# Kernel optimization log

Hardware: AMD Instinct MI355X
Metric: run time of the kernel (lower is better)

The kernel has to match this reference:

```python
import jax, jax.numpy as jnp
import numpy as np

N_NODES = 20000
N_EDGES = 320000
N_GRAPHS = 32
IN_CH = 5
HID = 64
HEADS = 4
DH = HID // HEADS  # 16
LAYERS = 8
EPS = 1e-5
SLOPE = 0.2


def setup_inputs() -> dict:
    key = jax.random.key(0)
    ks = jax.random.split(key, 32)
    inp = {}
    inp['x1'] = jax.random.normal(ks[0], (N_NODES, IN_CH), dtype=jnp.float32)
    inp['x2'] = jax.random.normal(ks[1], (N_NODES, IN_CH), dtype=jnp.float32)
    inp['edge_index1'] = jax.random.randint(ks[2], (2, N_EDGES), 0, N_NODES, dtype=jnp.int32)
    inp['edge_index2'] = jax.random.randint(ks[3], (2, N_EDGES), 0, N_NODES, dtype=jnp.int32)
    inp['batch1'] = jnp.sort(jax.random.randint(ks[4], (N_NODES,), 0, N_GRAPHS, dtype=jnp.int32))
    inp['batch2'] = jnp.sort(jax.random.randint(ks[5], (N_NODES,), 0, N_GRAPHS, dtype=jnp.int32))
    # node_lin
    inp['Wn'] = jax.random.normal(ks[6], (IN_CH, HID), dtype=jnp.float32) / np.sqrt(IN_CH)
    inp['bnode'] = jnp.zeros((HID,), dtype=jnp.float32)
    # GATv2 layers (stacked over LAYERS)
    s = 1.0 / np.sqrt(HID)
    inp['Wl'] = jax.random.normal(ks[7], (LAYERS, HID, HID), dtype=jnp.float32) * s
    inp['bl'] = jnp.zeros((LAYERS, HID), dtype=jnp.float32)
    inp['Wr'] = jax.random.normal(ks[8], (LAYERS, HID, HID), dtype=jnp.float32) * s
    inp['br'] = jnp.zeros((LAYERS, HID), dtype=jnp.float32)
    inp['att'] = jax.random.normal(ks[9], (LAYERS, HEADS, DH), dtype=jnp.float32) / np.sqrt(DH)
    inp['cbias'] = jnp.zeros((LAYERS, HID), dtype=jnp.float32)
    # batch norms
    inp['gamma'] = jnp.ones((LAYERS, HID), dtype=jnp.float32)
    inp['beta'] = jnp.zeros((LAYERS, HID), dtype=jnp.float32)
    # fc head
    inp['f1w'] = jax.random.normal(ks[10], (2 * HID, 256), dtype=jnp.float32) / np.sqrt(2 * HID)
    inp['f1b'] = jnp.zeros((256,), dtype=jnp.float32)
    inp['f2w'] = jax.random.normal(ks[11], (256, 128), dtype=jnp.float32) / np.sqrt(256)
    inp['f2b'] = jnp.zeros((128,), dtype=jnp.float32)
    inp['f3w'] = jax.random.normal(ks[12], (128, 1), dtype=jnp.float32) / np.sqrt(128)
    inp['f3b'] = jnp.zeros((1,), dtype=jnp.float32)
    return inp


def _gatv2_layer(x, src, dst, Wl, bl, Wr, br, att, bias):
    # x: [N, HID]; src/dst: [E'] (self loops included)
    N = x.shape[0]
    xl = (x @ Wl + bl).reshape(N, HEADS, DH)  # source transform
    xr = (x @ Wr + br).reshape(N, HEADS, DH)  # target transform
    e = jax.nn.leaky_relu(xl[src] + xr[dst], SLOPE)          # [E, H, DH]
    score = jnp.einsum('ehd,hd->eh', e, att)                  # [E, H]
    smax = jax.ops.segment_max(score, dst, num_segments=N)    # [N, H]
    ex = jnp.exp(score - smax[dst])
    denom = jax.ops.segment_sum(ex, dst, num_segments=N)
    alpha = ex / denom[dst]                                   # [E, H]
    msg = alpha[:, :, None] * xl[src]                         # [E, H, DH]
    out = jax.ops.segment_sum(msg, dst, num_segments=N)       # [N, H, DH]
    return out.reshape(N, HID) + bias


def _forward_once(x, edge_index, batch, Wn, bnode, Wl, bl, Wr, br, att, cbias, gamma, beta):
    N = x.shape[0]
    loop = jnp.arange(N, dtype=edge_index.dtype)
    src = jnp.concatenate([edge_index[0], loop])  # add_self_loops=True
    dst = jnp.concatenate([edge_index[1], loop])
    h = x @ Wn + bnode
    for l in range(LAYERS):
        g = _gatv2_layer(h, src, dst, Wl[l], bl[l], Wr[l], br[l], att[l], cbias[l])
        mu = g.mean(axis=0)
        var = g.var(axis=0)
        g = (g - mu) / jnp.sqrt(var + EPS) * gamma[l] + beta[l]
        h = h + jax.nn.elu(g)
    # global_mean_pool
    sums = jax.ops.segment_sum(h, batch, num_segments=N_GRAPHS)
    cnt = jax.ops.segment_sum(jnp.ones((N,), dtype=h.dtype), batch, num_segments=N_GRAPHS)
    return sums / jnp.maximum(cnt, 1.0)[:, None]


def reference(x1, edge_index1, batch1, x2, edge_index2, batch2, Wn, bnode, Wl, bl, Wr, br, att, cbias, gamma, beta, f1w, f1b, f2w, f2b, f3w, f3b):
    o1 = _forward_once(x1, edge_index1, batch1, Wn, bnode, Wl, bl, Wr, br, att, cbias, gamma, beta)
    o2 = _forward_once(x2, edge_index2, batch2, Wn, bnode, Wl, bl, Wr, br, att, cbias, gamma, beta)
    c = jnp.concatenate([o1, o2], axis=1)           # [G, 128]
    h = jax.nn.relu(c @ f1w + f1b)                   # dropout = identity (eval)
    h = jax.nn.relu(h @ f2w + f2b)
    return h @ f3w + f3b                             # [G, 1]
```

## Files before the change

### kernel.cpp

```cpp
#include <hip/hip_runtime.h>
#include <hip/hip_bf16.h>

#define N_NODES 20000
#define HID 64
#define EPS 1e-5f

struct GP {
    const int* ei;
    const int* batch;
    const float* x;
    int* deg;
    int* cursor;
    int* csr;
    float* h;
    float* xl;
    float* xr;
    float* gb;
    float* stats;
    float* osum;
};


__global__ void k_csr_init(GP a, GP b, int n, int two) {
    int t = blockIdx.x * blockDim.x + threadIdx.x;
    if (t < n) {
        a.deg[t] = 1;
        if (two) b.deg[t] = 1;
    }
}

__global__ void k_count(GP a, GP b, int Ea, int Eb, int two) {
    int t = blockIdx.x * blockDim.x + threadIdx.x;
    if (t < Ea) atomicAdd(&a.deg[a.ei[Ea + t]], 1);
    if (two && t < Eb) atomicAdd(&b.deg[b.ei[Eb + t]], 1);
}

#define SCAN_T 1024
#define SCAN_C 20
__global__ __launch_bounds__(1024) void k_scan(GP a, GP b, int n, int totA, int totB) {
    GP g = blockIdx.x ? b : a;
    int total = blockIdx.x ? totB : totA;
    __shared__ int sd[SCAN_T];
    int t = threadIdx.x;
    int base = t * SCAN_C;
    int loc[SCAN_C];
    int s = 0;
#pragma unroll
    for (int i = 0; i < SCAN_C; ++i) {
        int idx = base + i;
        loc[i] = (idx < n) ? g.deg[idx] : 0;
        s += loc[i];
    }
    sd[t] = s;
    __syncthreads();
    for (int off = 1; off < SCAN_T; off <<= 1) {
        int v = (t >= off) ? sd[t - off] : 0;
        __syncthreads();
        sd[t] += v;
        __syncthreads();
    }
    int run = sd[t] - s;
#pragma unroll
    for (int i = 0; i < SCAN_C; ++i) {
        int idx = base + i;
        if (idx < n) { g.deg[idx] = run; g.cursor[idx] = run; run += loc[i]; }
    }
    if (t == 0) g.deg[n] = total;
}

__global__ void k_scatter(GP a, GP b, int Ea, int Eb, int n, int two) {
    int t = blockIdx.x * blockDim.x + threadIdx.x;
    if (t < Ea) {
        int s = a.ei[t], d = a.ei[Ea + t];
        a.csr[atomicAdd(&a.cursor[d], 1)] = s;
    } else if (t < Ea + n) {
        int nn = t - Ea;
        a.csr[atomicAdd(&a.cursor[nn], 1)] = nn;
    }
    if (two) {
        if (t < Eb) {
            int s = b.ei[t], d = b.ei[Eb + t];
            b.csr[atomicAdd(&b.cursor[d], 1)] = s;
        } else if (t < Eb + n) {
            int nn = t - Eb;
            b.csr[atomicAdd(&b.cursor[nn], 1)] = nn;
        }
    }
}


__global__ void k_nodelin(GP a, GP b, int nPer, const float* __restrict__ Wn,
                          const float* __restrict__ bn, int n) {
    int bid = blockIdx.x;
    GP g = a;
    if (bid >= nPer) { g = b; bid -= nPer; }
    int idx = bid * 256 + threadIdx.x;
    if (idx >= n * HID) return;
    int node = idx >> 6, c = idx & 63;
    float acc = bn[c];
#pragma unroll
    for (int k = 0; k < 5; ++k) acc += g.x[node * 5 + k] * Wn[k * HID + c];
    g.h[idx] = acc;
}


__global__ __launch_bounds__(256) void k_lin2(GP ga, GP gbp, int nPer, int n,
        const float* __restrict__ Wl, const float* __restrict__ bl,
        const float* __restrict__ Wr, const float* __restrict__ br,
        const float* __restrict__ gamma, const float* __restrict__ beta, int layer) {
    __shared__ float wls[4096], wrs[4096];
    __shared__ float hs[1024];
    int bid = blockIdx.x;
    GP g = ga;
    if (bid >= nPer) { g = gbp; bid -= nPer; }
    for (int i = threadIdx.x; i < 4096; i += 256) { wls[i] = Wl[i]; wrs[i] = Wr[i]; }
    int c = threadIdx.x & 63;
    int wid = threadIdx.x >> 6;
    float blv = bl[c], brv = br[c];
    float mu = 0.f, inv = 1.f, gam = 1.f, bet = 0.f;
    if (layer > 0) {
        const float* st = g.stats + (layer - 1) * 128;
        float invn = 1.0f / (float)n;
        mu = st[c] * invn;
        float var = st[64 + c] * invn - mu * mu;
        inv = rsqrtf(fmaxf(var, 0.f) + EPS);
        gam = gamma[c]; bet = beta[c];
    }
    int stride = nPer * 16;
    for (int base = bid * 16; base < n; base += stride) {
        int nb = base + wid * 4;
        size_t off = (size_t)nb * 64 + c;
        float h0, h1, h2, h3;
        if (layer > 0) {
            float g0 = g.gb[off], g1 = g.gb[off + 64], g2 = g.gb[off + 128], g3 = g.gb[off + 192];
            float o0 = g.h[off], o1 = g.h[off + 64], o2 = g.h[off + 128], o3 = g.h[off + 192];
            float v0 = (g0 - mu) * inv * gam + bet; v0 = v0 > 0.f ? v0 : expm1f(v0);
            float v1 = (g1 - mu) * inv * gam + bet; v1 = v1 > 0.f ? v1 : expm1f(v1);
            float v2 = (g2 - mu) * inv * gam + bet; v2 = v2 > 0.f ? v2 : expm1f(v2);
            float v3 = (g3 - mu) * inv * gam + bet; v3 = v3 > 0.f ? v3 : expm1f(v3);
            h0 = o0 + v0; h1 = o1 + v1; h2 = o2 + v2; h3 = o3 + v3;
            g.h[off] = h0; g.h[off + 64] = h1; g.h[off + 128] = h2; g.h[off + 192] = h3;
        } else {
            h0 = g.h[off]; h1 = g.h[off + 64]; h2 = g.h[off + 128]; h3 = g.h[off + 192];
        }
        hs[wid * 256 + c] = h0;
        hs[wid * 256 + 64 + c] = h1;
        hs[wid * 256 + 128 + c] = h2;
        hs[wid * 256 + 192 + c] = h3;
        __syncthreads();
        float al0 = blv, al1 = blv, al2 = blv, al3 = blv;
        float ar0 = brv, ar1 = brv, ar2 = brv, ar3 = brv;
        const float* hw = &hs[wid * 256];
#pragma unroll 8
        for (int k = 0; k < 64; ++k) {
            float wl = wls[k * 64 + c], wr = wrs[k * 64 + c];
            float q0 = hw[k], q1 = hw[64 + k], q2 = hw[128 + k], q3 = hw[192 + k];
            al0 += q0 * wl; ar0 += q0 * wr;
            al1 += q1 * wl; ar1 += q1 * wr;
            al2 += q2 * wl; ar2 += q2 * wr;
            al3 += q3 * wl; ar3 += q3 * wr;
        }
        g.xl[off] = al0; g.xl[off + 64] = al1; g.xl[off + 128] = al2; g.xl[off + 192] = al3;
        g.xr[off] = ar0; g.xr[off + 64] = ar1; g.xr[off + 128] = ar2; g.xr[off + 192] = ar3;
        __syncthreads();
    }
}


__device__ __forceinline__ float red16(float p) {
    p += __int_as_float(__builtin_amdgcn_update_dpp(0, __float_as_int(p), 0xB1, 0xF, 0xF, true));
    p += __int_as_float(__builtin_amdgcn_update_dpp(0, __float_as_int(p), 0x4E, 0xF, 0xF, true));
    p += __int_as_float(__builtin_amdgcn_update_dpp(0, __float_as_int(p), 0x141, 0xF, 0xF, true));
    p += __int_as_float(__builtin_amdgcn_update_dpp(0, __float_as_int(p), 0x140, 0xF, 0xF, true));
    return p;
}

__device__ __forceinline__ void upd(float p, float xls, float& m, float& lsum, float& acc) {
    float mn = fmaxf(m, p);
    float sc = __expf(m - mn);
    float wv = __expf(p - mn);
    lsum = lsum * sc + wv;
    acc = acc * sc + wv * xls;
    m = mn;
}

__global__ __launch_bounds__(1024) void k_attn(GP ga, GP gbp, int nPer,
        const float* __restrict__ att, const float* __restrict__ cbias, int layer, int n) {
    int bid = blockIdx.x;
    GP g = ga;
    if (bid >= nPer) { g = gbp; bid -= nPer; }
    int lane = threadIdx.x & 63;
    int wid = threadIdx.x >> 6;
    int gw = bid * 16 + wid;
    int nw = nPer * 16;
    float attv = att[lane];
    float cb = cbias[lane];
    const int* __restrict__ rowptr = g.deg;
    const int* __restrict__ csr = g.csr;
    const float* __restrict__ xl = g.xl;
    const float* __restrict__ xr = g.xr;
    float* __restrict__ gbuf = g.gb;
    float* st = g.stats + layer * 128;
    float bsum = 0.f, bsq = 0.f;
    for (int node = gw; node < n; node += nw) {
        int start = rowptr[node], end = rowptr[node + 1];
        float xrv = xr[(size_t)node * 64 + lane];
        float m = -1e30f, lsum = 0.f, acc = 0.f;
        int idx = start;
        for (; idx + 4 <= end; idx += 4) {
            int s0 = csr[idx], s1 = csr[idx + 1], s2 = csr[idx + 2], s3 = csr[idx + 3];
            float x0 = xl[(size_t)s0 * 64 + lane];
            float x1 = xl[(size_t)s1 * 64 + lane];
            float x2 = xl[(size_t)s2 * 64 + lane];
            float x3 = xl[(size_t)s3 * 64 + lane];
            float e0 = x0 + xrv; e0 = e0 > 0.f ? e0 : 0.2f * e0;
            float e1 = x1 + xrv; e1 = e1 > 0.f ? e1 : 0.2f * e1;
            float e2 = x2 + xrv; e2 = e2 > 0.f ? e2 : 0.2f * e2;
            float e3 = x3 + xrv; e3 = e3 > 0.f ? e3 : 0.2f * e3;
            float p0 = red16(e0 * attv);
            float p1 = red16(e1 * attv);
            float p2 = red16(e2 * attv);
            float p3 = red16(e3 * attv);
            upd(p0, x0, m, lsum, acc);
            upd(p1, x1, m, lsum, acc);
            upd(p2, x2, m, lsum, acc);
            upd(p3, x3, m, lsum, acc);
        }
        for (; idx < end; ++idx) {
            int s0 = csr[idx];
            float x0 = xl[(size_t)s0 * 64 + lane];
            float e0 = x0 + xrv; e0 = e0 > 0.f ? e0 : 0.2f * e0;
            float p0 = red16(e0 * attv);
            upd(p0, x0, m, lsum, acc);
        }
        float outv = acc / lsum + cb;
        gbuf[(size_t)node * 64 + lane] = outv;
        bsum += outv; bsq += outv * outv;
    }
    __shared__ float sred[1024];
    sred[threadIdx.x] = bsum;
    __syncthreads();
    if (threadIdx.x < 64) {
        float t = 0.f;
#pragma unroll
        for (int w = 0; w < 16; ++w) t += sred[w * 64 + threadIdx.x];
        atomicAdd(&st[threadIdx.x], t);
    }
    __syncthreads();
    sred[threadIdx.x] = bsq;
    __syncthreads();
    if (threadIdx.x < 64) {
        float t = 0.f;
#pragma unroll
        for (int w = 0; w < 16; ++w) t += sred[w * 64 + threadIdx.x];
        atomicAdd(&st[64 + threadIdx.x], t);
    }
}


__global__ __launch_bounds__(256) void k_pool(GP ga, GP gbp, int nPer,
        const float* __restrict__ gamma, const float* __restrict__ beta, int n) {
    int bid = blockIdx.x;
    GP g = ga;
    if (bid >= nPer) { g = gbp; bid -= nPer; }
    int lane = threadIdx.x & 63, w = threadIdx.x >> 6;
    const float* st = g.stats + 7 * 128;
    float invn = 1.f / (float)n;
    float mu = st[lane] * invn;
    float var = st[64 + lane] * invn - mu * mu;
    float inv = rsqrtf(fmaxf(var, 0.f) + EPS);
    float gam = gamma[lane], bet = beta[lane];
    int chunk = (n + nPer - 1) / nPer;
    int s = bid * chunk;
    int e = min(s + chunk, n);
    float acc = 0.f;
    int cur = -1;
    for (int node = s + w; node < e; node += 4) {
        int bg = g.batch[node];
        size_t off = (size_t)node * 64 + lane;
        float gv = g.gb[off];
        float hv = g.h[off];
        float v = (gv - mu) * inv * gam + bet;
        float hn = hv + (v > 0.f ? v : expm1f(v));
        if (bg != cur) {
            if (cur >= 0) atomicAdd(&g.osum[cur * 64 + lane], acc);
            acc = 0.f; cur = bg;
        }
        acc += hn;
    }
    if (cur >= 0) atomicAdd(&g.osum[cur * 64 + lane], acc);
}


__device__ __forceinline__ int lb(const int* __restrict__ b, int n, int v) {
    int lo = 0, hi = n;
    while (lo < hi) { int mid = (lo + hi) >> 1; if (b[mid] < v) lo = mid + 1; else hi = mid; }
    return lo;
}

__global__ __launch_bounds__(256) void k_fc(const float* __restrict__ o1, const float* __restrict__ o2,
                                            const int* __restrict__ b1, const int* __restrict__ b2,
                                            const float* __restrict__ f1w, const float* __restrict__ f1b,
                                            const float* __restrict__ f2w, const float* __restrict__ f2b,
                                            const float* __restrict__ f3w, const float* __restrict__ f3b,
                                            float* __restrict__ out, int n) {
    int gid = blockIdx.x, t = threadIdx.x;
    __shared__ float cin[128];
    __shared__ float h1[256];
    __shared__ float red[128];
    __shared__ int cnts[2];
    if (t == 0) cnts[0] = lb(b1, n, gid + 1) - lb(b1, n, gid);
    if (t == 1) cnts[1] = lb(b2, n, gid + 1) - lb(b2, n, gid);
    __syncthreads();
    if (t < 64) {
        float c1 = (float)(cnts[0] > 0 ? cnts[0] : 1);
        float c2 = (float)(cnts[1] > 0 ? cnts[1] : 1);
        cin[t] = o1[gid * 64 + t] / c1;
        cin[64 + t] = o2[gid * 64 + t] / c2;
    }
    __syncthreads();
    float a = f1b[t];
#pragma unroll 8
    for (int k = 0; k < 128; ++k) a += cin[k] * f1w[k * 256 + t];
    h1[t] = fmaxf(a, 0.f);
    __syncthreads();
    if (t < 128) {
        float a2 = f2b[t];
#pragma unroll 8
        for (int k = 0; k < 256; ++k) a2 += h1[k] * f2w[k * 128 + t];
        red[t] = fmaxf(a2, 0.f) * f3w[t];
    }
    __syncthreads();
    for (int off = 64; off > 0; off >>= 1) {
        if (t < off) red[t] += red[t + off];
        __syncthreads();
    }
    if (t == 0) out[gid] = red[0] + f3b[0];
}


extern "C" void kernel_launch(void* const* d_in, const int* in_sizes, int n_in,
                              void* d_out, int out_size, void* d_ws, size_t ws_size,
                              hipStream_t stream) {
    const float* x1 = (const float*)d_in[0];
    const float* x2 = (const float*)d_in[1];
    const int* ei1 = (const int*)d_in[2];
    const int* ei2 = (const int*)d_in[3];
    const int* b1 = (const int*)d_in[4];
    const int* b2 = (const int*)d_in[5];
    const float* Wn = (const float*)d_in[6];
    const float* bnode = (const float*)d_in[7];
    const float* Wl = (const float*)d_in[8];
    const float* bl = (const float*)d_in[9];
    const float* Wr = (const float*)d_in[10];
    const float* br = (const float*)d_in[11];
    const float* att = (const float*)d_in[12];
    const float* cbias = (const float*)d_in[13];
    const float* gamma = (const float*)d_in[14];
    const float* beta = (const float*)d_in[15];
    const float* f1w = (const float*)d_in[16];
    const float* f1b = (const float*)d_in[17];
    const float* f2w = (const float*)d_in[18];
    const float* f2b = (const float*)d_in[19];
    const float* f3w = (const float*)d_in[20];
    const float* f3b = (const float*)d_in[21];
    float* out = (float*)d_out;

    const int N = N_NODES;
    const int EA = in_sizes[2] / 2;
    const int EB = in_sizes[3] / 2;
    const size_t INT_PG = 20096 + 20096 + 340096;
    const size_t BIG = (size_t)N * 64;
    const size_t SMALL = 2 * 1024 + 2 * 2048;
    const size_t dualBytes = 2 * INT_PG * 4 + (8 * BIG + SMALL) * 4;
    const int dual = (ws_size >= dualBytes) ? 1 : 0;

    int* ibase = (int*)d_ws;
    int* iA = ibase;
    int* iB = dual ? ibase + INT_PG : ibase;
    float* fbase = (float*)(ibase + (size_t)(dual ? 2 : 1) * INT_PG);
    float* hA = fbase;
    float* xlA = hA + BIG;
    float* xrA = xlA + BIG;
    float* gbA = xrA + BIG;
    float* hB = dual ? gbA + BIG : hA;
    float* xlB = dual ? hB + BIG : xlA;
    float* xrB = dual ? xlB + BIG : xrA;
    float* gbB = dual ? xrB + BIG : gbA;
    float* small = dual ? gbB + BIG : gbA + BIG;
    float* statsA = small;
    float* statsB = small + 1024;
    float* osumA = small + 2048;
    float* osumB = small + 4096;

    GP A, B;
    A.ei = ei1; A.batch = b1; A.x = x1;
    A.deg = iA; A.cursor = iA + 20096; A.csr = iA + 40192;
    A.h = hA; A.xl = xlA; A.xr = xrA; A.gb = gbA; A.stats = statsA; A.osum = osumA;
    B.ei = ei2; B.batch = b2; B.x = x2;
    B.deg = iB; B.cursor = iB + 20096; B.csr = iB + 40192;
    B.h = hB; B.xl = xlB; B.xr = xrB; B.gb = gbB; B.stats = statsB; B.osum = osumB;

    hipMemsetAsync(small, 0, SMALL * sizeof(float), stream);

    const int LIN2_NB = 625;
    const int ATT_NB = 256;
    const int POOL_NB = 250;

    if (dual) {
        int Emax = EA > EB ? EA : EB;
        k_csr_init<<<(N + 255) / 256, 256, 0, stream>>>(A, B, N, 1);
        k_count<<<(Emax + 255) / 256, 256, 0, stream>>>(A, B, EA, EB, 1);
        k_scan<<<2, 1024, 0, stream>>>(A, B, N, EA + N, EB + N);
        k_scatter<<<(Emax + N + 255) / 256, 256, 0, stream>>>(A, B, EA, EB, N, 1);
        k_nodelin<<<2 * ((N * 64) / 256), 256, 0, stream>>>(A, B, (N * 64) / 256, Wn, bnode, N);
        for (int l = 0; l < 8; ++l) {
            const float* gm = l ? gamma + (l - 1) * 64 : gamma;
            const float* bt = l ? beta + (l - 1) * 64 : beta;
            k_lin2<<<2 * LIN2_NB, 256, 0, stream>>>(A, B, LIN2_NB, N, Wl + l * 4096, bl + l * 64,
                                                    Wr + l * 4096, br + l * 64, gm, bt, l);
            k_attn<<<2 * ATT_NB, 1024, 0, stream>>>(A, B, ATT_NB, att + l * 64, cbias + l * 64, l, N);
        }
        k_pool<<<2 * POOL_NB, 256, 0, stream>>>(A, B, POOL_NB, gamma + 7 * 64, beta + 7 * 64, N);
    } else {
        for (int gi = 0; gi < 2; ++gi) {
            GP G = gi ? B : A;
            int E = gi ? EB : EA;
            k_csr_init<<<(N + 255) / 256, 256, 0, stream>>>(G, G, N, 0);
            k_count<<<(E + 255) / 256, 256, 0, stream>>>(G, G, E, E, 0);
            k_scan<<<1, 1024, 0, stream>>>(G, G, N, E + N, E + N);
            k_scatter<<<(E + N + 255) / 256, 256, 0, stream>>>(G, G, E, E, N, 0);
            k_nodelin<<<(N * 64) / 256, 256, 0, stream>>>(G, G, (N * 64) / 256, Wn, bnode, N);
            for (int l = 0; l < 8; ++l) {
                const float* gm = l ? gamma + (l - 1) * 64 : gamma;
                const float* bt = l ? beta + (l - 1) * 64 : beta;
                k_lin2<<<LIN2_NB, 256, 0, stream>>>(G, G, LIN2_NB, N, Wl + l * 4096, bl + l * 64,
                                                    Wr + l * 4096, br + l * 64, gm, bt, l);
                k_attn<<<ATT_NB, 1024, 0, stream>>>(G, G, ATT_NB, att + l * 64, cbias + l * 64, l, N);
            }
            k_pool<<<POOL_NB, 256, 0, stream>>>(G, G, POOL_NB, gamma + 7 * 64, beta + 7 * 64, N);
        }
    }
    k_fc<<<32, 256, 0, stream>>>(osumA, osumB, b1, b2, f1w, f1b, f2w, f2b, f3w, f3b, out, N);
}
```

Baseline: 749.0 us.

## Replace online softmax with self-loop-anchored exp and retile the lin2 GEMM

In the attention kernel, the running-max online softmax is replaced by a fixed shift: the self-loop score is computed first and every edge weight is exp(min(p - s_self, 80)). This removes the per-edge rescale exps and max tracking, leaving one exp per edge. It risks overflow or precision loss if scores run far above the self score, which the clamp at 80 only partly covers. LeakyReLU is folded into a select between att and 0.2*att. Separately, the linear kernel now does 8 nodes per wave with float4 LDS reads of h and fma accumulation, uses vectorized weight loads, drops the trailing barrier, and launches half as many blocks.

New measurement: 710.7 us. 5.1% less time.

```diff
diff --git a/kernel.cpp b/kernel.cpp
--- a/kernel.cpp
+++ b/kernel.cpp
@@ -109,11 +109,17 @@
         const float* __restrict__ Wr, const float* __restrict__ br,
         const float* __restrict__ gamma, const float* __restrict__ beta, int layer) {
     __shared__ float wls[4096], wrs[4096];
-    __shared__ float hs[1024];
+    __shared__ float hs[2048];
     int bid = blockIdx.x;
     GP g = ga;
     if (bid >= nPer) { g = gbp; bid -= nPer; }
-    for (int i = threadIdx.x; i < 4096; i += 256) { wls[i] = Wl[i]; wrs[i] = Wr[i]; }
+    {
+        const float4* wl4 = (const float4*)Wl;
+        const float4* wr4 = (const float4*)Wr;
+        float4* l4 = (float4*)wls;
+        float4* r4 = (float4*)wrs;
+        for (int i = threadIdx.x; i < 1024; i += 256) { l4[i] = wl4[i]; r4[i] = wr4[i]; }
+    }
     int c = threadIdx.x & 63;
     int wid = threadIdx.x >> 6;
     float blv = bl[c], brv = br[c];
@@ -126,43 +132,53 @@
         inv = rsqrtf(fmaxf(var, 0.f) + EPS);
         gam = gamma[c]; bet = beta[c];
     }
-    int stride = nPer * 16;
-    for (int base = bid * 16; base < n; base += stride) {
-        int nb = base + wid * 4;
-        size_t off = (size_t)nb * 64 + c;
-        float h0, h1, h2, h3;
+    float* hw = &hs[wid * 512];
+    const float4* hw4 = (const float4*)hw;
+    for (int base = bid * 32; base < n; base += nPer * 32) {
+        int nb = base + wid * 8;
+        size_t off0 = (size_t)nb * 64 + c;
+        float hv[8];
         if (layer > 0) {
-            float g0 = g.gb[off], g1 = g.gb[off + 64], g2 = g.gb[off + 128], g3 = g.gb[off + 192];
-            float o0 = g.h[off], o1 = g.h[off + 64], o2 = g.h[off + 128], o3 = g.h[off + 192];
-            float v0 = (g0 - mu) * inv * gam + bet; v0 = v0 > 0.f ? v0 : expm1f(v0);
-            float v1 = (g1 - mu) * inv * gam + bet; v1 = v1 > 0.f ? v1 : expm1f(v1);
-            float v2 = (g2 - mu) * inv * gam + bet; v2 = v2 > 0.f ? v2 : expm1f(v2);
-            float v3 = (g3 - mu) * inv * gam + bet; v3 = v3 > 0.f ? v3 : expm1f(v3);
-            h0 = o0 + v0; h1 = o1 + v1; h2 = o2 + v2; h3 = o3 + v3;
-            g.h[off] = h0; g.h[off + 64] = h1; g.h[off + 128] = h2; g.h[off + 192] = h3;
+#pragma unroll
+            for (int j = 0; j < 8; ++j) {
+                float gv = g.gb[off0 + j * 64];
+                float ov = g.h[off0 + j * 64];
+                float v = (gv - mu) * inv * gam + bet;
+                v = v > 0.f ? v : expm1f(v);
+                hv[j] = ov + v;
+                g.h[off0 + j * 64] = hv[j];
+            }
         } else {
-            h0 = g.h[off]; h1 = g.h[off + 64]; h2 = g.h[off + 128]; h3 = g.h[off + 192];
-        }
-        hs[wid * 256 + c] = h0;
-        hs[wid * 256 + 64 + c] = h1;
-        hs[wid * 256 + 128 + c] = h2;
-        hs[wid * 256 + 192 + c] = h3;
+#pragma unroll
+            for (int j = 0; j < 8; ++j) hv[j] = g.h[off0 + j * 64];
+        }
+#pragma unroll
+        for (int j = 0; j < 8; ++j) hw[j * 64 + c] = hv[j];
         __syncthreads();
-        float al0 = blv, al1 = blv, al2 = blv, al3 = blv;
-        float ar0 = brv, ar1 = brv, ar2 = brv, ar3 = brv;
-        const float* hw = &hs[wid * 256];
-#pragma unroll 8
-        for (int k = 0; k < 64; ++k) {
-            float wl = wls[k * 64 + c], wr = wrs[k * 64 + c];
-            float q0 = hw[k], q1 = hw[64 + k], q2 = hw[128 + k], q3 = hw[192 + k];
-            al0 += q0 * wl; ar0 += q0 * wr;
-            al1 += q1 * wl; ar1 += q1 * wr;
-            al2 += q2 * wl; ar2 += q2 * wr;
-            al3 += q3 * wl; ar3 += q3 * wr;
-        }
-        g.xl[off] = al0; g.xl[off + 64] = al1; g.xl[off + 128] = al2; g.xl[off + 192] = al3;
-        g.xr[off] = ar0; g.xr[off + 64] = ar1; g.xr[off + 128] = ar2; g.xr[off + 192] = ar3;
-        __syncthreads();
+        float accl[8], accr[8];
+#pragma unroll
+        for (int j = 0; j < 8; ++j) { accl[j] = blv; accr[j] = brv; }
+        for (int k4 = 0; k4 < 16; ++k4) {
+            float4 hq[8];
+#pragma unroll
+            for (int j = 0; j < 8; ++j) hq[j] = hw4[j * 16 + k4];
+#pragma unroll
+            for (int kk = 0; kk < 4; ++kk) {
+                float wl = wls[(k4 * 4 + kk) * 64 + c];
+                float wr = wrs[(k4 * 4 + kk) * 64 + c];
+#pragma unroll
+                for (int j = 0; j < 8; ++j) {
+                    float hx = (&hq[j].x)[kk];
+                    accl[j] = fmaf(hx, wl, accl[j]);
+                    accr[j] = fmaf(hx, wr, accr[j]);
+                }
+            }
+        }
+#pragma unroll
+        for (int j = 0; j < 8; ++j) {
+            g.xl[off0 + j * 64] = accl[j];
+            g.xr[off0 + j * 64] = accr[j];
+        }
     }
 }
 
@@ -173,15 +189,6 @@
     p += __int_as_float(__builtin_amdgcn_update_dpp(0, __float_as_int(p), 0x141, 0xF, 0xF, true));
     p += __int_as_float(__builtin_amdgcn_update_dpp(0, __float_as_int(p), 0x140, 0xF, 0xF, true));
     return p;
-}
-
-__device__ __forceinline__ void upd(float p, float xls, float& m, float& lsum, float& acc) {
-    float mn = fmaxf(m, p);
-    float sc = __expf(m - mn);
-    float wv = __expf(p - mn);
-    lsum = lsum * sc + wv;
-    acc = acc * sc + wv * xls;
-    m = mn;
 }
 
 __global__ __launch_bounds__(1024) void k_attn(GP ga, GP gbp, int nPer,
@@ -194,6 +201,7 @@
     int gw = bid * 16 + wid;
     int nw = nPer * 16;
     float attv = att[lane];
+    float attv2 = attv * 0.2f;
     float cb = cbias[lane];
     const int* __restrict__ rowptr = g.deg;
     const int* __restrict__ csr = g.csr;
@@ -205,7 +213,9 @@
     for (int node = gw; node < n; node += nw) {
         int start = rowptr[node], end = rowptr[node + 1];
         float xrv = xr[(size_t)node * 64 + lane];
-        float m = -1e30f, lsum = 0.f, acc = 0.f;
+        float ts = xl[(size_t)node * 64 + lane] + xrv;
+        float sself = red16(ts * (ts > 0.f ? attv : attv2));
+        float lsum = 0.f, acc = 0.f;
         int idx = start;
         for (; idx + 4 <= end; idx += 4) {
             int s0 = csr[idx], s1 = csr[idx + 1], s2 = csr[idx + 2], s3 = csr[idx + 3];
@@ -213,25 +223,29 @@
             float x1 = xl[(size_t)s1 * 64 + lane];
             float x2 = xl[(size_t)s2 * 64 + lane];
             float x3 = xl[(size_t)s3 * 64 + lane];
-            float e0 = x0 + xrv; e0 = e0 > 0.f ? e0 : 0.2f * e0;
-            float e1 = x1 + xrv; e1 = e1 > 0.f ? e1 : 0.2f * e1;
-            float e2 = x2 + xrv; e2 = e2 > 0.f ? e2 : 0.2f * e2;
-            float e3 = x3 + xrv; e3 = e3 > 0.f ? e3 : 0.2f * e3;
-            float p0 = red16(e0 * attv);
-            float p1 = red16(e1 * attv);
-            float p2 = red16(e2 * attv);
-            float p3 = red16(e3 * attv);
-            upd(p0, x0, m, lsum, acc);
-            upd(p1, x1, m, lsum, acc);
-            upd(p2, x2, m, lsum, acc);
-            upd(p3, x3, m, lsum, acc);
+            float t0 = x0 + xrv, t1 = x1 + xrv, t2 = x2 + xrv, t3 = x3 + xrv;
+            float p0 = red16(t0 * (t0 > 0.f ? attv : attv2));
+            float p1 = red16(t1 * (t1 > 0.f ? attv : attv2));
+            float p2 = red16(t2 * (t2 > 0.f ? attv : attv2));
+            float p3 = red16(t3 * (t3 > 0.f ? attv : attv2));
+            float w0 = __expf(fminf(p0 - sself, 80.f));
+            float w1 = __expf(fminf(p1 - sself, 80.f));
+            float w2 = __expf(fminf(p2 - sself, 80.f));
+            float w3 = __expf(fminf(p3 - sself, 80.f));
+            lsum += (w0 + w1) + (w2 + w3);
+            acc = fmaf(w0, x0, acc);
+            acc = fmaf(w1, x1, acc);
+            acc = fmaf(w2, x2, acc);
+            acc = fmaf(w3, x3, acc);
         }
         for (; idx < end; ++idx) {
             int s0 = csr[idx];
             float x0 = xl[(size_t)s0 * 64 + lane];
-            float e0 = x0 + xrv; e0 = e0 > 0.f ? e0 : 0.2f * e0;
-            float p0 = red16(e0 * attv);
-            upd(p0, x0, m, lsum, acc);
+            float t0 = x0 + xrv;
+            float p0 = red16(t0 * (t0 > 0.f ? attv : attv2));
+            float w0 = __expf(fminf(p0 - sself, 80.f));
+            lsum += w0;
+            acc = fmaf(w0, x0, acc);
         }
         float outv = acc / lsum + cb;
         gbuf[(size_t)node * 64 + lane] = outv;
@@ -403,7 +417,7 @@
 
     hipMemsetAsync(small, 0, SMALL * sizeof(float), stream);
 
-    const int LIN2_NB = 625;
+    const int LIN2_NB = 320;
     const int ATT_NB = 256;
     const int POOL_NB = 250;
 
```
